# Kernel optimization log

Hardware: AMD Instinct MI355X
Metric: run time of the kernel (lower is better)

## Reference

```python
import jax, jax.numpy as jnp
import numpy as np

N_NODES = 50000
N_EDGES = 800000
IN_FT = 256
OUT_FT = 128


def setup_inputs() -> dict:
    key = jax.random.key(0)
    k_seq, k_src, k_dst, k_val, k_w = jax.random.split(key, 5)
    seq = jax.random.normal(k_seq, (N_NODES, IN_FT), dtype=jnp.float32)
    edge_src = jax.random.randint(k_src, (N_EDGES,), 0, N_NODES, dtype=jnp.int64)
    edge_dst = jax.random.randint(k_dst, (N_EDGES,), 0, N_NODES, dtype=jnp.int64)
    edge_val = jax.random.uniform(k_val, (N_EDGES,), dtype=jnp.float32)
    # xavier_uniform for Linear(in_ft, out_ft): limit = sqrt(6/(in+out))
    limit = float(np.sqrt(6.0 / (IN_FT + OUT_FT)))
    W = jax.random.uniform(k_w, (OUT_FT, IN_FT), minval=-limit, maxval=limit, dtype=jnp.float32)
    bias = jnp.zeros((OUT_FT,), dtype=jnp.float32)
    prelu_a = jnp.full((1,), 0.25, dtype=jnp.float32)  # nn.PReLU default slope
    return {"seq": seq, "edge_src": edge_src, "edge_dst": edge_dst,
            "edge_val": edge_val, "W": W, "bias": bias, "prelu_a": prelu_a}


def reference(seq, edge_src, edge_dst, edge_val, W, bias, prelu_a):
    # seq_fts = fc(seq): [N, out_ft]
    seq_fts = jnp.einsum('ni,oi->no', seq, W)
    # sparse spmm: out[dst] += val * seq_fts[src]
    msgs = seq_fts[edge_src] * edge_val[:, None]          # [E, out_ft]
    out = jax.ops.segment_sum(msgs, edge_dst, num_segments=seq.shape[0])
    out = out + bias                                       # bias add
    # PReLU with learnable slope a
    return jnp.where(out >= 0, out, prelu_a * out)
```

## Files before the change

kernel.cpp:

```cpp
#include <hip/hip_runtime.h>
#include <hip/hip_bf16.h>

#define N_NODES 50000
#define N_EDGES 800000
#define IN_FT 256
#define OUT_FT 128

typedef __bf16 bf16;
typedef __attribute__((ext_vector_type(8))) __bf16 bf16x8;
typedef __attribute__((ext_vector_type(4))) __bf16 bf16x4;
typedef __attribute__((ext_vector_type(4))) float floatx4;

static __device__ inline unsigned short f2bf_bits(float f) {
    unsigned u = __float_as_uint(f);
    return (unsigned short)((u + 0x7FFFu + ((u >> 16) & 1u)) >> 16);
}

#define BKN 128
#define NBUCK 392
#define NPAD (NBUCK * BKN)
#define EPB 2048
#define NBLK_A ((N_EDGES + EPB - 1) / EPB)
#define CELL 32
#define SXCAP 2560
#define GM 128
#define GEMM_BLKS ((N_NODES + GM - 1) / GM)
#define WP 264
#define SMEM_BYTES (128 * WP * 2)

__global__ __launch_bounds__(512) void k_ga(const float* __restrict__ seq,
                                            const float* __restrict__ W,
                                            unsigned short* __restrict__ seq_fts,
                                            const int* __restrict__ src,
                                            const int* __restrict__ dst,
                                            const float* __restrict__ val,
                                            int* __restrict__ cnt,
                                            uint2* __restrict__ part) {
    const int t = threadIdx.x;
    __shared__ __align__(16) char smem[SMEM_BYTES];
    if (blockIdx.x < GEMM_BLKS) {
        bf16* Wlds = (bf16*)smem;
        {
            const int row = t >> 2, c0 = (t & 3) * 64;
            const float* wsrc = W + row * IN_FT + c0;
            bf16* dstp = Wlds + row * WP + c0;
#pragma unroll
            for (int c = 0; c < 16; ++c) {
                float4 v = *(const float4*)(wsrc + c * 4);
                bf16x4 o = {(bf16)v.x, (bf16)v.y, (bf16)v.z, (bf16)v.w};
                *(bf16x4*)(dstp + c * 4) = o;
            }
        }
        const int lane = t & 63;
        const int wave = t >> 6;
        const int quad = lane >> 4;
        const int l16  = lane & 15;

        int arow = blockIdx.x * GM + wave * 16 + l16;
        if (arow >= N_NODES) arow = 0;
        const float* ap = seq + (size_t)arow * IN_FT + quad * 8;
        bf16x8 afr[8];
#pragma unroll
        for (int s = 0; s < 8; ++s) {
            float4 v0 = *(const float4*)(ap + s * 32);
            float4 v1 = *(const float4*)(ap + s * 32 + 4);
            bf16x8 a;
            a[0] = (bf16)v0.x; a[1] = (bf16)v0.y; a[2] = (bf16)v0.z; a[3] = (bf16)v0.w;
            a[4] = (bf16)v1.x; a[5] = (bf16)v1.y; a[6] = (bf16)v1.z; a[7] = (bf16)v1.w;
            afr[s] = a;
        }
        __syncthreads();

        const int mbase = blockIdx.x * GM + wave * 16;
#pragma unroll
        for (int h = 0; h < 2; ++h) {
            floatx4 acc[4];
#pragma unroll
            for (int q = 0; q < 4; ++q) acc[q] = (floatx4){0.f, 0.f, 0.f, 0.f};
#pragma unroll
            for (int s = 0; s < 8; ++s) {
#pragma unroll
                for (int q = 0; q < 4; ++q) {
                    const int tt = h * 4 + q;
                    bf16x8 bfr = *(const bf16x8*)(Wlds + (tt * 16 + l16) * WP + quad * 8 + s * 32);
                    acc[q] = __builtin_amdgcn_mfma_f32_16x16x32_bf16(afr[s], bfr, acc[q], 0, 0, 0);
                }
            }
#pragma unroll
            for (int q = 0; q < 4; ++q) {
                const int tt = h * 4 + q;
#pragma unroll
                for (int r = 0; r < 4; ++r) {
                    int m = mbase + quad * 4 + r;
                    if (m < N_NODES)
                        seq_fts[(size_t)m * OUT_FT + tt * 16 + l16] = f2bf_bits(acc[q][r]);
                }
            }
        }
    } else {
        int*   h     = (int*)smem;
        int*   lbase = h + NBUCK;
        int*   sc    = lbase + NBUCK;
        uint2* srt   = (uint2*)(sc + 512);

        const int B2 = blockIdx.x - GEMM_BLKS;
        const int e0 = B2 * EPB;
        if (t < NBUCK) h[t] = 0;
        __syncthreads();

        int      myd[4];
        int      myofs[4];
        unsigned myx[4];
#pragma unroll
        for (int k = 0; k < 4; ++k) {
            int e = e0 + k * 512 + t;
            int d = (e < N_EDGES) ? dst[e] : -1;
            myd[k] = d;
            if (d >= 0) {
                myx[k] = (unsigned)(unsigned short)src[e]
                       | ((unsigned)f2bf_bits(val[e]) << 16);
                myofs[k] = atomicAdd(&h[d >> 7], 1);
            }
        }
        __syncthreads();
        int v = (t < NBUCK) ? min(h[t], CELL) : 0;
        sc[t] = v;
        __syncthreads();
        for (int s = 1; s < 512; s <<= 1) {
            int a = (t >= s) ? sc[t - s] : 0;
            __syncthreads();
            sc[t] += a;
            __syncthreads();
        }
        if (t < NBUCK) { lbase[t] = sc[t] - v; cnt[t * NBLK_A + B2] = v; }
        __syncthreads();
        const int total = sc[NBUCK - 1];
#pragma unroll
        for (int k = 0; k < 4; ++k) {
            int d = myd[k];
            if (d >= 0 && myofs[k] < CELL)
                srt[lbase[d >> 7] + myofs[k]] = make_uint2(myx[k], (unsigned)d);
        }
        __syncthreads();
        for (int i = t; i < total; i += 512) {
            uint2 r = srt[i];
            int bb = (int)(r.y >> 7);
            part[(size_t)(bb * NBLK_A + B2) * CELL + (unsigned)(i - lbase[bb])] = r;
        }
    }
}

#define NW 16
__global__ __launch_bounds__(1024) void k_BG(const int* __restrict__ cnt,
                                             const uint2* __restrict__ part,
                                             const unsigned* __restrict__ fts,
                                             const float* __restrict__ bias,
                                             const float* __restrict__ prelu_a,
                                             float* __restrict__ out) {
    const int b = blockIdx.x, t = threadIdx.x;
    __shared__ int sc[1024];
    __shared__ int ncnt[BKN], nbase[BKN], ncur[BKN];
    __shared__ int tot_sh;
    __shared__ unsigned fx[SXCAP];
    __shared__ unsigned char fdn[SXCAP];
    __shared__ unsigned sx[SXCAP];

    if (t < BKN) ncnt[t] = 0;
    const int len = (t < NBLK_A) ? cnt[b * NBLK_A + t] : 0;
    sc[t] = len;
    __syncthreads();
    for (int s = 1; s < 512; s <<= 1) {
        int a = (t >= s) ? sc[t - s] : 0;
        __syncthreads();
        sc[t] += a;
        __syncthreads();
    }
    const int cellbase = sc[t] - len;
    if (t == NBLK_A - 1) tot_sh = sc[NBLK_A - 1];
    __syncthreads();
    const int tot  = tot_sh;
    const int totc = (tot < SXCAP) ? tot : SXCAP;

    if (t < NBLK_A) {
        const uint2* cp = part + (size_t)(b * NBLK_A + t) * CELL;
        for (int k = 0; k < len; ++k) {
            int idx = cellbase + k;
            if (idx < SXCAP) {
                uint2 r = cp[k];
                int dn = (int)(r.y & (BKN - 1));
                fx[idx] = r.x;
                fdn[idx] = (unsigned char)dn;
                atomicAdd(&ncnt[dn], 1);
            }
        }
    }
    __syncthreads();
    int v2 = (t < BKN) ? ncnt[t] : 0;
    if (t < BKN) sc[t] = v2;
    __syncthreads();
    for (int s = 1; s < BKN; s <<= 1) {
        int a = (t < BKN && t >= s) ? sc[t - s] : 0;
        __syncthreads();
        if (t < BKN) sc[t] += a;
        __syncthreads();
    }
    if (t < BKN) {
        nbase[t] = sc[t] - v2;
        ncur[t]  = sc[t] - v2;
    }
    __syncthreads();
    for (int i = t; i < totc; i += 1024) {
        unsigned x = fx[i];
        int dn = fdn[i];
        int j = atomicAdd(&ncur[dn], 1);
        sx[j] = x;
    }
    __syncthreads();

    const int wave = t >> 6;
    const int lane = t & 63;
    const float2 bb2 = *(const float2*)&bias[lane * 2];
    const float a = prelu_a[0];
    for (int ln = wave; ln < BKN; ln += NW) {
        const int n = b * BKN + ln;
        if (n >= N_NODES) continue;
        const int s0 = nbase[ln];
        const int s1 = s0 + ncnt[ln];
        float acc0 = 0.f, acc1 = 0.f;
        int j = s0;
        for (; j + 7 < s1; j += 8) {
            unsigned x0 = sx[j],     x1 = sx[j + 1];
            unsigned x2 = sx[j + 2], x3 = sx[j + 3];
            unsigned x4 = sx[j + 4], x5 = sx[j + 5];
            unsigned x6 = sx[j + 6], x7 = sx[j + 7];
            unsigned q0 = fts[(x0 & 0xFFFFu) * 64u + lane];
            unsigned q1 = fts[(x1 & 0xFFFFu) * 64u + lane];
            unsigned q2 = fts[(x2 & 0xFFFFu) * 64u + lane];
            unsigned q3 = fts[(x3 & 0xFFFFu) * 64u + lane];
            unsigned q4 = fts[(x4 & 0xFFFFu) * 64u + lane];
            unsigned q5 = fts[(x5 & 0xFFFFu) * 64u + lane];
            unsigned q6 = fts[(x6 & 0xFFFFu) * 64u + lane];
            unsigned q7 = fts[(x7 & 0xFFFFu) * 64u + lane];
            acc0 += __uint_as_float(x0 & 0xFFFF0000u) * __uint_as_float(q0 << 16);
            acc1 += __uint_as_float(x0 & 0xFFFF0000u) * __uint_as_float(q0 & 0xFFFF0000u);
            acc0 += __uint_as_float(x1 & 0xFFFF0000u) * __uint_as_float(q1 << 16);
            acc1 += __uint_as_float(x1 & 0xFFFF0000u) * __uint_as_float(q1 & 0xFFFF0000u);
            acc0 += __uint_as_float(x2 & 0xFFFF0000u) * __uint_as_float(q2 << 16);
            acc1 += __uint_as_float(x2 & 0xFFFF0000u) * __uint_as_float(q2 & 0xFFFF0000u);
            acc0 += __uint_as_float(x3 & 0xFFFF0000u) * __uint_as_float(q3 << 16);
            acc1 += __uint_as_float(x3 & 0xFFFF0000u) * __uint_as_float(q3 & 0xFFFF0000u);
            acc0 += __uint_as_float(x4 & 0xFFFF0000u) * __uint_as_float(q4 << 16);
            acc1 += __uint_as_float(x4 & 0xFFFF0000u) * __uint_as_float(q4 & 0xFFFF0000u);
            acc0 += __uint_as_float(x5 & 0xFFFF0000u) * __uint_as_float(q5 << 16);
            acc1 += __uint_as_float(x5 & 0xFFFF0000u) * __uint_as_float(q5 & 0xFFFF0000u);
            acc0 += __uint_as_float(x6 & 0xFFFF0000u) * __uint_as_float(q6 << 16);
            acc1 += __uint_as_float(x6 & 0xFFFF0000u) * __uint_as_float(q6 & 0xFFFF0000u);
            acc0 += __uint_as_float(x7 & 0xFFFF0000u) * __uint_as_float(q7 << 16);
            acc1 += __uint_as_float(x7 & 0xFFFF0000u) * __uint_as_float(q7 & 0xFFFF0000u);
        }
        for (; j + 3 < s1; j += 4) {
            unsigned x0 = sx[j],     x1 = sx[j + 1];
            unsigned x2 = sx[j + 2], x3 = sx[j + 3];
            unsigned q0 = fts[(x0 & 0xFFFFu) * 64u + lane];
            unsigned q1 = fts[(x1 & 0xFFFFu) * 64u + lane];
            unsigned q2 = fts[(x2 & 0xFFFFu) * 64u + lane];
            unsigned q3 = fts[(x3 & 0xFFFFu) * 64u + lane];
            acc0 += __uint_as_float(x0 & 0xFFFF0000u) * __uint_as_float(q0 << 16);
            acc1 += __uint_as_float(x0 & 0xFFFF0000u) * __uint_as_float(q0 & 0xFFFF0000u);
            acc0 += __uint_as_float(x1 & 0xFFFF0000u) * __uint_as_float(q1 << 16);
            acc1 += __uint_as_float(x1 & 0xFFFF0000u) * __uint_as_float(q1 & 0xFFFF0000u);
            acc0 += __uint_as_float(x2 & 0xFFFF0000u) * __uint_as_float(q2 << 16);
            acc1 += __uint_as_float(x2 & 0xFFFF0000u) * __uint_as_float(q2 & 0xFFFF0000u);
            acc0 += __uint_as_float(x3 & 0xFFFF0000u) * __uint_as_float(q3 << 16);
            acc1 += __uint_as_float(x3 & 0xFFFF0000u) * __uint_as_float(q3 & 0xFFFF0000u);
        }
        for (; j < s1; ++j) {
            unsigned x0 = sx[j];
            unsigned q0 = fts[(x0 & 0xFFFFu) * 64u + lane];
            float v0 = __uint_as_float(x0 & 0xFFFF0000u);
            acc0 += v0 * __uint_as_float(q0 << 16);
            acc1 += v0 * __uint_as_float(q0 & 0xFFFF0000u);
        }
        float x0f = acc0 + bb2.x;
        float x1f = acc1 + bb2.y;
        x0f = (x0f >= 0.f) ? x0f : a * x0f;
        x1f = (x1f >= 0.f) ? x1f : a * x1f;
        *(float2*)&out[(size_t)n * OUT_FT + lane * 2] = make_float2(x0f, x1f);
    }
}

extern "C" void kernel_launch(void* const* d_in, const int* in_sizes, int n_in,
                              void* d_out, int out_size, void* d_ws, size_t ws_size,
                              hipStream_t stream) {
    const float* seq      = (const float*)d_in[0];
    const int*   edge_src = (const int*)d_in[1];
    const int*   edge_dst = (const int*)d_in[2];
    const float* edge_val = (const float*)d_in[3];
    const float* W        = (const float*)d_in[4];
    const float* bias     = (const float*)d_in[5];
    const float* prelu_a  = (const float*)d_in[6];
    float* out = (float*)d_out;

    char* ws = (char*)d_ws;
    size_t off = 0;
    auto alloc = [&](size_t bytes) {
        void* p = ws + off;
        off = (off + bytes + 255) & ~(size_t)255;
        return p;
    };
    unsigned short* seq_fts = (unsigned short*)alloc((size_t)N_NODES * OUT_FT * sizeof(unsigned short));
    int*   cnt  = (int*)alloc((size_t)NBUCK * NBLK_A * sizeof(int));
    uint2* part = (uint2*)alloc((size_t)NBUCK * NBLK_A * CELL * sizeof(uint2));
    (void)ws_size; (void)in_sizes; (void)n_in; (void)out_size;

    k_ga<<<GEMM_BLKS + NBLK_A, 512, 0, stream>>>(seq, W, seq_fts,
                                                 edge_src, edge_dst, edge_val,
                                                 cnt, part);
    k_BG<<<NBUCK, 1024, 0, stream>>>(cnt, part, (const unsigned*)seq_fts,
                                     bias, prelu_a, out);
}
```

Measured before the change: 161.1 us.

## Halve GEMM LDS footprint and replace Hillis-Steele scans with wave-shuffle scans

```diff
diff --git a/kernel.cpp b/kernel.cpp
--- a/kernel.cpp
+++ b/kernel.cpp
@@ -18,7 +18,6 @@
 
 #define BKN 128
 #define NBUCK 392
-#define NPAD (NBUCK * BKN)
 #define EPB 2048
 #define NBLK_A ((N_EDGES + EPB - 1) / EPB)
 #define CELL 32
@@ -26,31 +25,46 @@
 #define GM 128
 #define GEMM_BLKS ((N_NODES + GM - 1) / GM)
 #define WP 264
-#define SMEM_BYTES (128 * WP * 2)
-
-__global__ __launch_bounds__(512) void k_ga(const float* __restrict__ seq,
-                                            const float* __restrict__ W,
-                                            unsigned short* __restrict__ seq_fts,
-                                            const int* __restrict__ src,
-                                            const int* __restrict__ dst,
-                                            const float* __restrict__ val,
-                                            int* __restrict__ cnt,
-                                            uint2* __restrict__ part) {
+#define SMEM_BYTES (64 * WP * 2)
+
+template<int NTHREADS>
+__device__ inline int blk_scan_incl(int v, int t, int* wsum) {
+    const int lane = t & 63;
+    const int w = t >> 6;
+#pragma unroll
+    for (int s = 1; s < 64; s <<= 1) {
+        int o = __shfl_up(v, s, 64);
+        if (lane >= s) v += o;
+    }
+    __syncthreads();
+    if (lane == 63) wsum[w] = v;
+    __syncthreads();
+    if (w == 0) {
+        constexpr int NWAVE = NTHREADS / 64;
+        int x = (lane < NWAVE) ? wsum[lane] : 0;
+#pragma unroll
+        for (int s = 1; s < NWAVE; s <<= 1) {
+            int o = __shfl_up(x, s, 64);
+            if (lane >= s) x += o;
+        }
+        if (lane < NWAVE) wsum[lane] = x;
+    }
+    __syncthreads();
+    return v + ((w > 0) ? wsum[w - 1] : 0);
+}
+
+__global__ __launch_bounds__(512, 6) void k_ga(const float* __restrict__ seq,
+                                               const float* __restrict__ W,
+                                               unsigned short* __restrict__ seq_fts,
+                                               const int* __restrict__ src,
+                                               const int* __restrict__ dst,
+                                               const float* __restrict__ val,
+                                               int* __restrict__ cnt,
+                                               uint2* __restrict__ part) {
     const int t = threadIdx.x;
     __shared__ __align__(16) char smem[SMEM_BYTES];
     if (blockIdx.x < GEMM_BLKS) {
         bf16* Wlds = (bf16*)smem;
-        {
-            const int row = t >> 2, c0 = (t & 3) * 64;
-            const float* wsrc = W + row * IN_FT + c0;
-            bf16* dstp = Wlds + row * WP + c0;
-#pragma unroll
-            for (int c = 0; c < 16; ++c) {
-                float4 v = *(const float4*)(wsrc + c * 4);
-                bf16x4 o = {(bf16)v.x, (bf16)v.y, (bf16)v.z, (bf16)v.w};
-                *(bf16x4*)(dstp + c * 4) = o;
-            }
-        }
         const int lane = t & 63;
         const int wave = t >> 6;
         const int quad = lane >> 4;
@@ -69,11 +83,24 @@
             a[4] = (bf16)v1.x; a[5] = (bf16)v1.y; a[6] = (bf16)v1.z; a[7] = (bf16)v1.w;
             afr[s] = a;
         }
-        __syncthreads();
 
         const int mbase = blockIdx.x * GM + wave * 16;
 #pragma unroll
-        for (int h = 0; h < 2; ++h) {
+        for (int h2 = 0; h2 < 2; ++h2) {
+            __syncthreads();
+            {
+                const int row = t >> 3;
+                const int c0 = (t & 7) * 32;
+                const float* wsrc = W + (size_t)(h2 * 64 + row) * IN_FT + c0;
+                bf16* dstp = Wlds + row * WP + c0;
+#pragma unroll
+                for (int c = 0; c < 8; ++c) {
+                    float4 vv = *(const float4*)(wsrc + c * 4);
+                    bf16x4 o = {(bf16)vv.x, (bf16)vv.y, (bf16)vv.z, (bf16)vv.w};
+                    *(bf16x4*)(dstp + c * 4) = o;
+                }
+            }
+            __syncthreads();
             floatx4 acc[4];
 #pragma unroll
             for (int q = 0; q < 4; ++q) acc[q] = (floatx4){0.f, 0.f, 0.f, 0.f};
@@ -81,27 +108,28 @@
             for (int s = 0; s < 8; ++s) {
 #pragma unroll
                 for (int q = 0; q < 4; ++q) {
-                    const int tt = h * 4 + q;
-                    bf16x8 bfr = *(const bf16x8*)(Wlds + (tt * 16 + l16) * WP + quad * 8 + s * 32);
+                    bf16x8 bfr = *(const bf16x8*)(Wlds + (q * 16 + l16) * WP + quad * 8 + s * 32);
                     acc[q] = __builtin_amdgcn_mfma_f32_16x16x32_bf16(afr[s], bfr, acc[q], 0, 0, 0);
                 }
             }
 #pragma unroll
             for (int q = 0; q < 4; ++q) {
-                const int tt = h * 4 + q;
+                const int col = (h2 * 4 + q) * 16 + l16;
 #pragma unroll
                 for (int r = 0; r < 4; ++r) {
                     int m = mbase + quad * 4 + r;
                     if (m < N_NODES)
-                        seq_fts[(size_t)m * OUT_FT + tt * 16 + l16] = f2bf_bits(acc[q][r]);
+                        seq_fts[(size_t)m * OUT_FT + col] = f2bf_bits(acc[q][r]);
                 }
             }
         }
     } else {
-        int*   h     = (int*)smem;
-        int*   lbase = h + NBUCK;
-        int*   sc    = lbase + NBUCK;
-        uint2* srt   = (uint2*)(sc + 512);
+        int*   ib    = (int*)smem;
+        int*   h     = ib;
+        int*   lbase = ib + 392;
+        int*   wsum  = ib + 784;
+        int*   totp  = ib + 792;
+        uint2* srt   = (uint2*)(smem + 3200);
 
         const int B2 = blockIdx.x - GEMM_BLKS;
         const int e0 = B2 * EPB;
@@ -123,18 +151,12 @@
             }
         }
         __syncthreads();
-        int v = (t < NBUCK) ? min(h[t], CELL) : 0;
-        sc[t] = v;
+        const int v = (t < NBUCK) ? min(h[t], CELL) : 0;
+        const int inc = blk_scan_incl<512>(v, t, wsum);
+        if (t < NBUCK) { lbase[t] = inc - v; cnt[t * NBLK_A + B2] = v; }
+        if (t == 511) *totp = inc;
         __syncthreads();
-        for (int s = 1; s < 512; s <<= 1) {
-            int a = (t >= s) ? sc[t - s] : 0;
-            __syncthreads();
-            sc[t] += a;
-            __syncthreads();
-        }
-        if (t < NBUCK) { lbase[t] = sc[t] - v; cnt[t * NBLK_A + B2] = v; }
-        __syncthreads();
-        const int total = sc[NBUCK - 1];
+        const int total = *totp;
 #pragma unroll
         for (int k = 0; k < 4; ++k) {
             int d = myd[k];
@@ -158,28 +180,20 @@
                                              const float* __restrict__ prelu_a,
                                              float* __restrict__ out) {
     const int b = blockIdx.x, t = threadIdx.x;
-    __shared__ int sc[1024];
+    __shared__ int wsum[16];
+    __shared__ int tot_sh;
     __shared__ int ncnt[BKN], nbase[BKN], ncur[BKN];
-    __shared__ int tot_sh;
     __shared__ unsigned fx[SXCAP];
     __shared__ unsigned char fdn[SXCAP];
     __shared__ unsigned sx[SXCAP];
 
     if (t < BKN) ncnt[t] = 0;
     const int len = (t < NBLK_A) ? cnt[b * NBLK_A + t] : 0;
-    sc[t] = len;
-    __syncthreads();
-    for (int s = 1; s < 512; s <<= 1) {
-        int a = (t >= s) ? sc[t - s] : 0;
-        __syncthreads();
-        sc[t] += a;
-        __syncthreads();
-    }
-    const int cellbase = sc[t] - len;
-    if (t == NBLK_A - 1) tot_sh = sc[NBLK_A - 1];
-    __syncthreads();
-    const int tot  = tot_sh;
-    const int totc = (tot < SXCAP) ? tot : SXCAP;
+    const int inc = blk_scan_incl<1024>(len, t, wsum);
+    const int cellbase = inc - len;
+    if (t == 1023) tot_sh = inc;
+    __syncthreads();
+    const int totc = (tot_sh < SXCAP) ? tot_sh : SXCAP;
 
     if (t < NBLK_A) {
         const uint2* cp = part + (size_t)(b * NBLK_A + t) * CELL;
@@ -195,18 +209,11 @@
         }
     }
     __syncthreads();
-    int v2 = (t < BKN) ? ncnt[t] : 0;
-    if (t < BKN) sc[t] = v2;
-    __syncthreads();
-    for (int s = 1; s < BKN; s <<= 1) {
-        int a = (t < BKN && t >= s) ? sc[t - s] : 0;
-        __syncthreads();
-        if (t < BKN) sc[t] += a;
-        __syncthreads();
-    }
+    const int v2 = (t < BKN) ? ncnt[t] : 0;
+    const int inc2 = blk_scan_incl<1024>(v2, t, wsum);
     if (t < BKN) {
-        nbase[t] = sc[t] - v2;
-        ncur[t]  = sc[t] - v2;
+        nbase[t] = inc2 - v2;
+        ncur[t]  = inc2 - v2;
     }
     __syncthreads();
     for (int i = t; i < totc; i += 1024) {
```

Result: no change. 159.6 us (-1.0%).
